# Optimization experiments

Hardware: AMD Instinct MI355X
Metric: run time of the kernel (lower is better)

## Reference

```python
import jax, jax.numpy as jnp
import numpy as np

DIM = 512
H = 48
W = 48
WS = 6
NH = 16
HEAD = DIM // NH
SCALE = HEAD ** -0.5
MLP_RATIO = 4
EPS = 1e-3  # keras LayerNormalization default epsilon
B = 16
L = H * W
M = WS * WS
NW = (H // WS) * (W // WS)


def _rel_pos_index(ws):
    # replicates tf.meshgrid (indexing='xy') construction exactly
    ch = np.arange(ws)
    cw = np.arange(ws)
    coords = np.stack(np.meshgrid(ch, cw))              # (2, ws, ws)
    cf = coords.reshape(2, -1)                          # (2, M)
    cf1 = np.concatenate([cf, np.zeros((2, 1), cf.dtype)], axis=1)  # (2, M+1) with global (0,0)
    rel = cf[:, :, None] - cf1[:, None, :]              # (2, M, M+1)
    rel = rel.transpose(1, 2, 0).copy()
    rel[:, :, 0] += ws - 1
    rel[:, :, 1] += ws - 1
    rel[:, :, 0] *= 2 * ws - 1
    return rel.sum(-1)                                  # (M, M+1)

REL_IDX = jnp.asarray(_rel_pos_index(WS))


def layernorm(x, g, b):
    m = x.mean(-1, keepdims=True)
    v = ((x - m) ** 2).mean(-1, keepdims=True)
    return (x - m) / jnp.sqrt(v + EPS) * g + b


def setup_inputs() -> dict:
    key = jax.random.key(0)
    ks = jax.random.split(key, 8)
    dense = lambda k, i, o: jax.random.normal(k, (i, o), jnp.float32) * (1.0 / np.sqrt(i))
    return dict(
        x=jax.random.normal(ks[0], (B, L, DIM), jnp.float32),
        xavg=jax.random.normal(ks[1], (B, 1, DIM), jnp.float32),
        w_kv=dense(ks[2], DIM, 2 * DIM), b_kv=jnp.zeros((2 * DIM,), jnp.float32),
        w_q=dense(ks[3], DIM, DIM), b_q=jnp.zeros((DIM,), jnp.float32),
        rel_bias_table=jax.random.normal(ks[4], ((2 * WS - 1) ** 2, NH), jnp.float32) * 0.02,
        g1=jnp.ones((DIM,), jnp.float32), be1=jnp.zeros((DIM,), jnp.float32),
        g2=jnp.ones((DIM,), jnp.float32), be2=jnp.zeros((DIM,), jnp.float32),
        w_fc1=dense(ks[5], DIM, MLP_RATIO * DIM), b_fc1=jnp.zeros((MLP_RATIO * DIM,), jnp.float32),
        w_fc2=dense(ks[6], MLP_RATIO * DIM, DIM), b_fc2=jnp.zeros((DIM,), jnp.float32),
    )


def _heads(t):
    # (B*, N, C) -> (B*, NH, N, HEAD)
    return t.reshape(t.shape[0], t.shape[1], NH, HEAD).transpose(0, 2, 1, 3)


def _forward(x, xavg, w_kv, b_kv, w_q, b_q, rel_bias_table, g1, be1, g2, be2,
             w_fc1, b_fc1, w_fc2, b_fc2):
    shortcut, shortcut_avg = x, xavg
    xn = layernorm(x, g1, be1)                          # (B, L, C)
    xavgn = layernorm(xavg, g1, be1)                    # (B, 1, C)

    # window partition: (B, L, C) -> (B*NW, M, C)
    xw = xn.reshape(B, H // WS, WS, W // WS, WS, DIM)
    xw = xw.transpose(0, 1, 3, 2, 4, 5).reshape(B * NW, M, DIM)

    # per-window tokens + repeated global token as keys/values
    xavgR = jnp.repeat(xavgn, NW, axis=0)               # (B*NW, 1, C), batch-major like tf.repeat
    x_c = jnp.concatenate([xw, xavgR], axis=1)          # (B*NW, M+1, C)

    kv = x_c @ w_kv + b_kv                              # (B*NW, M+1, 2C)
    q = xw @ w_q + b_q                                  # (B*NW, M, C)
    q_avg = xavgn @ w_q + b_q                           # (B, 1, C)
    kv_g = xn @ w_kv + b_kv                             # (B, L, 2C)

    k, v = jnp.split(kv, 2, axis=-1)
    kg, vg = jnp.split(kv_g, 2, axis=-1)

    qh = _heads(q) * SCALE                              # (B*NW, NH, M, HEAD)
    attn = jnp.einsum('bhqd,bhkd->bhqk', qh, _heads(k))  # (B*NW, NH, M, M+1)
    bias = rel_bias_table[REL_IDX.reshape(-1)].reshape(M, M + 1, NH)
    attn = attn + bias.transpose(2, 0, 1)[None]
    attn = jax.nn.softmax(attn, axis=-1)
    xo = jnp.einsum('bhqk,bhkd->bhqd', attn, _heads(v))
    xo = xo.transpose(0, 2, 1, 3).reshape(B * NW, M, DIM)

    # global token attends to all tokens
    qg = _heads(q_avg) * SCALE                          # (B, NH, 1, HEAD)
    attng = jax.nn.softmax(jnp.einsum('bhqd,bhkd->bhqk', qg, _heads(kg)), axis=-1)
    xavg_o = jnp.einsum('bhqk,bhkd->bhqd', attng, _heads(vg))
    xavg_o = xavg_o.transpose(0, 2, 1, 3).reshape(B, 1, DIM)

    # window reverse: (B*NW, M, C) -> (B, L, C)
    xr = xo.reshape(B, H // WS, W // WS, WS, WS, DIM)
    xr = xr.transpose(0, 1, 3, 2, 4, 5).reshape(B, L, DIM)

    x = shortcut + xr
    xavg = shortcut_avg + xavg_o

    mlp = lambda t: jax.nn.gelu(t @ w_fc1 + b_fc1, approximate=False) @ w_fc2 + b_fc2
    x = x + mlp(layernorm(x, g2, be2))
    xavg = xavg + mlp(layernorm(xavg, g2, be2))
    return x, xavg


def reference(x, xavg, w_kv, b_kv, w_q, b_q, rel_bias_table, g1, be1, g2, be2,
              w_fc1, b_fc1, w_fc2, b_fc2):
    return _forward(x, xavg, w_kv, b_kv, w_q, b_q, rel_bias_table, g1, be1, g2, be2,
                    w_fc1, b_fc1, w_fc2, b_fc2)
```

## Files before the change

kernel.cpp:

```cpp
#include <hip/hip_runtime.h>
#include <stdint.h>

#define DIM 512
#define NHEAD 16
#define HEADD 32
#define BATCH 16
#define SEQL 2304
#define XROWS (BATCH*SEQL)
#define NROWS (XROWS + BATCH)
#define ATT_SCALE 0.17677669529663687f

typedef __attribute__((ext_vector_type(8))) short short8;
typedef __attribute__((ext_vector_type(4))) float f32x4;

__device__ __forceinline__ float bf2f(unsigned short v) {
    union { unsigned u; float f; } t; t.u = ((unsigned)v) << 16; return t.f;
}
__device__ __forceinline__ unsigned short f2bf(float f) {
    union { float f; unsigned u; } t; t.f = f;
    unsigned r = t.u + 0x7fffu + ((t.u >> 16) & 1u);
    return (unsigned short)(r >> 16);
}
__device__ __forceinline__ void unpack8(const int4 c, float* o) {
    union { unsigned u; float f; } t;
    unsigned w0 = (unsigned)c.x, w1 = (unsigned)c.y, w2 = (unsigned)c.z, w3 = (unsigned)c.w;
    t.u = w0 << 16;         o[0] = t.f;
    t.u = w0 & 0xffff0000u; o[1] = t.f;
    t.u = w1 << 16;         o[2] = t.f;
    t.u = w1 & 0xffff0000u; o[3] = t.f;
    t.u = w2 << 16;         o[4] = t.f;
    t.u = w2 & 0xffff0000u; o[5] = t.f;
    t.u = w3 << 16;         o[6] = t.f;
    t.u = w3 & 0xffff0000u; o[7] = t.f;
}
__device__ __forceinline__ void gl_lds16(const void* g, void* l) {
    __builtin_amdgcn_global_load_lds((const __attribute__((address_space(1))) unsigned int*)g,
                                     (__attribute__((address_space(3))) unsigned int*)l,
                                     16, 0, 0);
}

__device__ __forceinline__ float gelu_exact(float v) {
    union { float f; unsigned u; } zc; zc.f = v * 0.70710678118654752f;
    unsigned sgn = zc.u & 0x80000000u;
    union { float f; unsigned u; } az; az.u = zc.u & 0x7fffffffu;
    float t  = __builtin_amdgcn_rcpf(fmaf(0.3275911f, az.f, 1.0f));
    float p  = t * fmaf(t, fmaf(t, fmaf(t, fmaf(t, 1.061405429f, -1.453152027f),
                                        1.421413741f), -0.284496736f), 0.254829592f);
    float e  = __expf(-az.f * az.f);
    union { float f; unsigned u; } er; er.f = fmaf(-p, e, 1.0f);
    er.u |= sgn;
    return 0.5f * v * (1.0f + er.f);
}

__device__ __forceinline__ void ln_row(const float* __restrict__ src, int lane,
                                       const float* __restrict__ g, const float* __restrict__ be,
                                       unsigned short* __restrict__ outrow) {
    int c0 = lane * 8;
    float4 v0 = *(const float4*)(src + c0);
    float4 v1 = *(const float4*)(src + c0 + 4);
    float s = v0.x+v0.y+v0.z+v0.w + v1.x+v1.y+v1.z+v1.w;
    float q = v0.x*v0.x+v0.y*v0.y+v0.z*v0.z+v0.w*v0.w + v1.x*v1.x+v1.y*v1.y+v1.z*v1.z+v1.w*v1.w;
    for (int m = 1; m < 64; m <<= 1) { s += __shfl_xor(s, m); q += __shfl_xor(q, m); }
    float mean = s * (1.0f/512.0f);
    float var  = q * (1.0f/512.0f) - mean*mean;
    float rs = rsqrtf(var + 1e-3f);
    float4 g0 = *(const float4*)(g + c0);
    float4 g1 = *(const float4*)(g + c0 + 4);
    float4 b0 = *(const float4*)(be + c0);
    float4 b1 = *(const float4*)(be + c0 + 4);
    unsigned short o[8];
    o[0] = f2bf((v0.x-mean)*rs*g0.x + b0.x);
    o[1] = f2bf((v0.y-mean)*rs*g0.y + b0.y);
    o[2] = f2bf((v0.z-mean)*rs*g0.z + b0.z);
    o[3] = f2bf((v0.w-mean)*rs*g0.w + b0.w);
    o[4] = f2bf((v1.x-mean)*rs*g1.x + b1.x);
    o[5] = f2bf((v1.y-mean)*rs*g1.y + b1.y);
    o[6] = f2bf((v1.z-mean)*rs*g1.z + b1.z);
    o[7] = f2bf((v1.w-mean)*rs*g1.w + b1.w);
    *(int4*)(outrow + c0) = *(const int4*)o;
}

#define TPOSE_BLKS 2816
#define SPACK_BLKS 90
#define LN1_BLKS   9220
__global__ __launch_bounds__(256) void prep_kernel(const float* __restrict__ w_q,
                                                   const float* __restrict__ w_kv,
                                                   const float* __restrict__ w_fc1,
                                                   const float* __restrict__ w_fc2,
                                                   unsigned short* __restrict__ Wqkv_t,
                                                   unsigned short* __restrict__ Wfc1_t,
                                                   unsigned short* __restrict__ Wfc2_t,
                                                   const float* __restrict__ b_q,
                                                   const float* __restrict__ b_kv,
                                                   const float* __restrict__ rel_table,
                                                   float* __restrict__ bqkv,
                                                   float* __restrict__ bias_exp,
                                                   const float* __restrict__ x,
                                                   const float* __restrict__ xavg,
                                                   const float* __restrict__ g1,
                                                   const float* __restrict__ be1,
                                                   unsigned short* __restrict__ xn) {
    __shared__ float tile[32][33];
    int blk = blockIdx.x;
    if (blk < TPOSE_BLKS) {
        int t = blk;
        const float* src; unsigned short* dst;
        int Kd, Nd, rowOff, tk;
        if (t < 256)        { src = w_q;   dst = Wqkv_t; Kd = 512;  Nd = 512;  rowOff = 0;   tk = 16; }
        else if (t < 768)   { t -= 256;  src = w_kv;  dst = Wqkv_t; Kd = 512;  Nd = 1024; rowOff = 512; tk = 16; }
        else if (t < 1792)  { t -= 768;  src = w_fc1; dst = Wfc1_t; Kd = 512;  Nd = 2048; rowOff = 0;   tk = 16; }
        else                { t -= 1792; src = w_fc2; dst = Wfc2_t; Kd = 2048; Nd = 512;  rowOff = 0;   tk = 64; }
        int k0 = (t % tk) * 32;
        int n0 = (t / tk) * 32;
        int tx = threadIdx.x & 31, ty = threadIdx.x >> 5;
        #pragma unroll
        for (int r = 0; r < 32; r += 8)
            tile[r + ty][tx] = src[(long)(k0 + r + ty) * Nd + n0 + tx];
        __syncthreads();
        #pragma unroll
        for (int r = 0; r < 32; r += 8)
            dst[(long)(rowOff + n0 + r + ty) * Kd + k0 + tx] = f2bf(tile[tx][r + ty]);
        return;
    }
    blk -= TPOSE_BLKS;
    if (blk < SPACK_BLKS) {
        int i = blk * 256 + threadIdx.x;
        if (i < 1536) { bqkv[i] = (i < 512) ? b_q[i] : b_kv[i - 512]; return; }
        i -= 1536;
        if (i < NHEAD*36*37) {
            int h = i / (36*37); int rem = i % (36*37); int qi = rem / 37; int j = rem % 37;
            int c0m = qi % 6, c1m = qi / 6;
            int c0n = (j < 36) ? (j % 6) : 0;
            int c1n = (j < 36) ? (j / 6) : 0;
            int id = (c0m - c0n + 5) * 11 + (c1m - c1n + 5);
            bias_exp[i] = rel_table[id * NHEAD + h];
        }
        return;
    }
    blk -= SPACK_BLKS;
    int wv = threadIdx.x >> 6, lane = threadIdx.x & 63;
    int r = blk * 4 + wv;
    if (r >= NROWS) return;
    const float* src = (r < XROWS) ? (x + (long)r * DIM) : (xavg + (long)(r - XROWS) * DIM);
    ln_row(src, lane, g1, be1, xn + (long)r * DIM);
}

__global__ __launch_bounds__(256) void ln_kernel(const float* __restrict__ p1,
                                                 const float* __restrict__ g, const float* __restrict__ be,
                                                 unsigned short* __restrict__ out, int nrows) {
    int wv = threadIdx.x >> 6, lane = threadIdx.x & 63;
    int r = blockIdx.x * 4 + wv;
    if (r >= nrows) return;
    ln_row(p1 + (long)r * DIM, lane, g, be, out + (long)r * DIM);
}

template<bool GELU_ACT, bool OUT_BF16, bool HAS_RES>
__global__ __launch_bounds__(256) void gemm_kernel(const short* __restrict__ A,
                                                   const short* __restrict__ Bt,
                                                   const float* __restrict__ bias,
                                                   void* __restrict__ Cout,
                                                   const float* __restrict__ Res,
                                                   int M, int N, int K, int nbx) {
    __shared__ short lds[2 * 128 * 64];
    short* lds_a = lds;
    short* lds_b = lds + 128 * 64;
    const int tid = threadIdx.x;
    const int lane = tid & 63;
    const int wv = tid >> 6;

    const int nwg = gridDim.x;
    const int orig = blockIdx.x;
    const int q = nwg >> 3, r = nwg & 7;
    const int xcd = orig & 7, lid = orig >> 3;
    const int wg = (xcd < r ? xcd * (q + 1) : r * (q + 1) + (xcd - r) * q) + lid;
    const int m0 = (wg / nbx) * 128;
    const int n0 = (wg % nbx) * 128;
    const int wm = (wv >> 1) * 64;
    const int wn = (wv & 1) * 64;

    f32x4 acc[4][4];
    #pragma unroll
    for (int i = 0; i < 4; i++)
        #pragma unroll
        for (int j = 0; j < 4; j++) { acc[i][j][0]=0.f; acc[i][j][1]=0.f; acc[i][j][2]=0.f; acc[i][j][3]=0.f; }

    const int srow = tid >> 3;
    const int msl  = (tid & 7) ^ (srow & 7);
    const short* Aa = A + (long)(m0 + srow) * K + msl * 8;
    const short* Bb = Bt + (long)(n0 + srow) * K + msl * 8;
    short* la = lds_a + tid * 8;
    short* lb = lds_b + tid * 8;

    const int quad = lane >> 4;
    const int l15 = lane & 15;
    const short* ra0 = lds_a + (wm + l15) * 64 + ((quad)     ^ (l15 & 7)) * 8;
    const short* ra1 = lds_a + (wm + l15) * 64 + ((4 + quad) ^ (l15 & 7)) * 8;
    const short* rb0 = lds_b + (wn + l15) * 64 + ((quad)     ^ (l15 & 7)) * 8;
    const short* rb1 = lds_b + (wn + l15) * 64 + ((4 + quad) ^ (l15 & 7)) * 8;

    for (int k0 = 0; k0 < K; k0 += 64) {
        __syncthreads();
        #pragma unroll
        for (int i = 0; i < 4; i++) {
            gl_lds16(Aa + (long)(i * 32) * K + k0, la + i * 256 * 8);
            gl_lds16(Bb + (long)(i * 32) * K + k0, lb + i * 256 * 8);
        }
        __syncthreads();
        short8 af[4], bf4[4];
        #pragma unroll
        for (int mt = 0; mt < 4; mt++) af[mt] = *(const short8*)(ra0 + mt * 16 * 64);
        #pragma unroll
        for (int nt = 0; nt < 4; nt++) bf4[nt] = *(const short8*)(rb0 + nt * 16 * 64);
        #pragma unroll
        for (int mt = 0; mt < 4; mt++)
            #pragma unroll
            for (int nt = 0; nt < 4; nt++)
                acc[mt][nt] = __builtin_amdgcn_mfma_f32_16x16x32_bf16(af[mt], bf4[nt], acc[mt][nt], 0, 0, 0);
        #pragma unroll
        for (int mt = 0; mt < 4; mt++) af[mt] = *(const short8*)(ra1 + mt * 16 * 64);
        #pragma unroll
        for (int nt = 0; nt < 4; nt++) bf4[nt] = *(const short8*)(rb1 + nt * 16 * 64);
        #pragma unroll
        for (int mt = 0; mt < 4; mt++)
            #pragma unroll
            for (int nt = 0; nt < 4; nt++)
                acc[mt][nt] = __builtin_amdgcn_mfma_f32_16x16x32_bf16(af[mt], bf4[nt], acc[mt][nt], 0, 0, 0);
    }

    float* ctile = (float*)lds;
    const int lrow_w = ((wv >> 1) << 4) + quad * 4;
    const int col_w  = ((wv & 1) << 6) + l15;
    const int lrow_r = tid >> 3;
    const int cg     = tid & 7;
    const int sub    = lrow_r & 15, half = lrow_r >> 4;
    float bv[16];
    #pragma unroll
    for (int i = 0; i < 4; i++)
        *(float4*)(bv + i * 4) = *(const float4*)(bias + n0 + cg * 16 + i * 4);

    #pragma unroll
    for (int mt = 0; mt < 4; mt++) {
        __syncthreads();
        #pragma unroll
        for (int nt = 0; nt < 4; nt++)
            #pragma unroll
            for (int r2 = 0; r2 < 4; r2++)
                ctile[(lrow_w + r2) * 132 + col_w + nt * 16] = acc[mt][nt][r2];
        __syncthreads();
        int grow = m0 + half * 64 + mt * 16 + sub;
        if (grow < M) {
            int gcol = n0 + cg * 16;
            float v[16];
            #pragma unroll
            for (int i = 0; i < 4; i++)
                *(float4*)(v + i * 4) = *(const float4*)(ctile + lrow_r * 132 + cg * 16 + i * 4);
            float rv[16];
            if (HAS_RES) {
                #pragma unroll
                for (int i = 0; i < 4; i++)
                    *(float4*)(rv + i * 4) = *(const float4*)(Res + (long)grow * N + gcol + i * 4);
            }
            if (OUT_BF16) {
                unsigned short ob[16];
                #pragma unroll
                for (int i = 0; i < 16; i++) {
                    float vv = v[i] + bv[i];
                    if (GELU_ACT) vv = gelu_exact(vv);
                    if (HAS_RES) vv += rv[i];
                    ob[i] = f2bf(vv);
                }
                unsigned short* dst = (unsigned short*)Cout + (long)grow * N + gcol;
                *(int4*)dst       = *(const int4*)ob;
                *(int4*)(dst + 8) = *(const int4*)(ob + 8);
            } else {
                float* dst = (float*)Cout + (long)grow * N + gcol;
                #pragma unroll
                for (int i = 0; i < 4; i++) {
                    float4 ov;
                    float* vp = v + i * 4;
                    float* rp = rv + i * 4;
                    ov.x = vp[0] + bv[i*4+0]; ov.y = vp[1] + bv[i*4+1];
                    ov.z = vp[2] + bv[i*4+2]; ov.w = vp[3] + bv[i*4+3];
                    if (GELU_ACT) { ov.x = gelu_exact(ov.x); ov.y = gelu_exact(ov.y);
                                    ov.z = gelu_exact(ov.z); ov.w = gelu_exact(ov.w); }
                    if (HAS_RES) { ov.x += rp[0]; ov.y += rp[1]; ov.z += rp[2]; ov.w += rp[3]; }
                    *(float4*)(dst + i * 4) = ov;
                }
            }
        }
    }
}

__global__ __launch_bounds__(256) void attn_kernel(const short* __restrict__ qkv,
                                                   const float* __restrict__ bias_exp,
                                                   const float* __restrict__ xin,
                                                   const float* __restrict__ xavg,
                                                   float* __restrict__ XALL) {
    __shared__ short vt[4][32 * 64];
    __shared__ short pl[4][48 * 64];
    __shared__ float sums[4][48];
    const int tid = threadIdx.x;
    if (blockIdx.x < 4096) {
        const int wv = tid >> 6;
        const int lane = tid & 63;
        const int gw = blockIdx.x * 4 + wv;
        const int win = gw >> 4;
        const int h = gw & 15;
        const int b = win >> 6;
        const int i1 = (win >> 3) & 7;
        const int i3 = win & 7;
        short* VT = vt[wv];
        short* PL = pl[wv];
        float* SM = sums[wv];
        const int quad = lane >> 4;
        const int l15 = lane & 15;

        {
            int4 z; z.x = 0; z.y = 0; z.z = 0; z.w = 0;
            int4* v4 = (int4*)VT;
            #pragma unroll
            for (int i = 0; i < 4; i++) v4[lane + 64 * i] = z;
            int4* p4 = (int4*)PL;
            #pragma unroll
            for (int i = 0; i < 6; i++) p4[lane + 64 * i] = z;
        }
        if (lane < 37) {
            long grow;
            if (lane < 36) { int i2 = lane / 6, i4 = lane % 6; grow = (long)b * SEQL + (i1*6 + i2) * 48 + i3*6 + i4; }
            else grow = XROWS + b;
            const int4* vp = (const int4*)(qkv + grow * 1536 + 1024 + h * 32);
            int4 r0 = vp[0], r1 = vp[1], r2v = vp[2], r3 = vp[3];
            const unsigned short* u0 = (const unsigned short*)&r0;
            const unsigned short* u1 = (const unsigned short*)&r1;
            const unsigned short* u2 = (const unsigned short*)&r2v;
            const unsigned short* u3 = (const unsigned short*)&r3;
            #pragma unroll
            for (int t = 0; t < 8; t++) VT[t * 64 + lane]        = (short)u0[t];
            #pragma unroll
            for (int t = 0; t < 8; t++) VT[(8 + t) * 64 + lane]  = (short)u1[t];
            #pragma unroll
            for (int t = 0; t < 8; t++) VT[(16 + t) * 64 + lane] = (short)u2[t];
            #pragma unroll
            for (int t = 0; t < 8; t++) VT[(24 + t) * 64 + lane] = (short)u3[t];
        }
        __syncthreads();

        short8 qf[3], kf[3];
        #pragma unroll
        for (int tm = 0; tm < 3; tm++) {
            int qi = tm * 16 + l15;
            if (qi < 36) {
                int i2 = qi / 6, i4 = qi % 6;
                long grow = (long)b * SEQL + (i1*6 + i2) * 48 + i3*6 + i4;
                qf[tm] = *(const short8*)(qkv + grow * 1536 + h * 32 + quad * 8);
            } else {
                #pragma unroll
                for (int i = 0; i < 8; i++) qf[tm][i] = 0;
            }
        }
        #pragma unroll
        for (int tn = 0; tn < 3; tn++) {
            int j = tn * 16 + l15;
            if (j <= 36) {
                long grow;
                if (j < 36) { int i2 = j / 6, i4 = j % 6; grow = (long)b * SEQL + (i1*6 + i2) * 48 + i3*6 + i4; }
                else grow = XROWS + b;
                kf[tn] = *(const short8*)(qkv + grow * 1536 + 512 + h * 32 + quad * 8);
            } else {
                #pragma unroll
                for (int i = 0; i < 8; i++) kf[tn][i] = 0;
            }
        }
        f32x4 s[3][3];
        #pragma unroll
        for (int tm = 0; tm < 3; tm++)
            #pragma unroll
            for (int tn = 0; tn < 3; tn++) {
                f32x4 z; z[0]=0.f; z[1]=0.f; z[2]=0.f; z[3]=0.f;
                s[tm][tn] = __builtin_amdgcn_mfma_f32_16x16x32_bf16(qf[tm], kf[tn], z, 0, 0, 0);
            }
        #pragma unroll
        for (int tm = 0; tm < 3; tm++)
            #pragma unroll
            for (int r = 0; r < 4; r++) {
                int qi = tm * 16 + quad * 4 + r;
                const float* bh = bias_exp + h * (36*37) + (qi < 36 ? qi : 35) * 37;
                #pragma unroll
                for (int tn = 0; tn < 3; tn++) {
                    int j = tn * 16 + l15;
                    float bv = bh[j <= 36 ? j : 36];
                    float v = fmaf(s[tm][tn][r], ATT_SCALE, bv);
                    s[tm][tn][r] = (j <= 36) ? v : -1e30f;
                }
            }
        #pragma unroll
        for (int tm = 0; tm < 3; tm++)
            #pragma unroll
            for (int r = 0; r < 4; r++) {
                float mx = fmaxf(fmaxf(s[tm][0][r], s[tm][1][r]), s[tm][2][r]);
                for (int m = 1; m < 16; m <<= 1) mx = fmaxf(mx, __shfl_xor(mx, m));
                float e0 = __expf(s[tm][0][r] - mx);
                float e1 = __expf(s[tm][1][r] - mx);
                float e2 = __expf(s[tm][2][r] - mx);
                float sum = e0 + e1 + e2;
                for (int m = 1; m < 16; m <<= 1) sum += __shfl_xor(sum, m);
                s[tm][0][r] = e0; s[tm][1][r] = e1; s[tm][2][r] = e2;
                if (l15 == 0) SM[tm * 16 + quad * 4 + r] = 1.0f / sum;
            }
        #pragma unroll
        for (int tm = 0; tm < 3; tm++)
            #pragma unroll
            for (int r = 0; r < 4; r++) {
                int row = (tm * 16 + quad * 4 + r) * 64;
                #pragma unroll
                for (int tn = 0; tn < 3; tn++)
                    PL[row + tn * 16 + l15] = (short)f2bf(s[tm][tn][r]);
            }
        f32x4 o[2][3];
        #pragma unroll
        for (int i = 0; i < 2; i++)
            #pragma unroll
            for (int j = 0; j < 3; j++) { o[i][j][0]=0.f; o[i][j][1]=0.f; o[i][j][2]=0.f; o[i][j][3]=0.f; }
        #pragma unroll
        for (int ch = 0; ch < 2; ch++) {
            short8 va[2], pb[3];
            #pragma unroll
            for (int tmd = 0; tmd < 2; tmd++)
                va[tmd] = *(const short8*)(VT + (tmd * 16 + l15) * 64 + ch * 32 + quad * 8);
            #pragma unroll
            for (int tnq = 0; tnq < 3; tnq++)
                pb[tnq] = *(const short8*)(PL + (tnq * 16 + l15) * 64 + ch * 32 + quad * 8);
            #pragma unroll
            for (int tmd = 0; tmd < 2; tmd++)
                #pragma unroll
                for (int tnq = 0; tnq < 3; tnq++)
                    o[tmd][tnq] = __builtin_amdgcn_mfma_f32_16x16x32_bf16(va[tmd], pb[tnq], o[tmd][tnq], 0, 0, 0);
        }
        #pragma unroll
        for (int tnq = 0; tnq < 3; tnq++) {
            int qi = tnq * 16 + l15;
            if (qi >= 36) continue;
            int i2 = qi / 6, i4 = qi % 6;
            long growq = (long)b * SEQL + (i1*6 + i2) * 48 + i3*6 + i4;
            float is = SM[qi];
            #pragma unroll
            for (int tmd = 0; tmd < 2; tmd++) {
                long base = growq * DIM + h * 32 + tmd * 16 + quad * 4;
                float4 xv = *(const float4*)(xin + base);
                float4 ov;
                ov.x = xv.x + o[tmd][tnq][0] * is;
                ov.y = xv.y + o[tmd][tnq][1] * is;
                ov.z = xv.z + o[tmd][tnq][2] * is;
                ov.w = xv.w + o[tmd][tnq][3] * is;
                *(float4*)(XALL + base) = ov;
            }
        }
        return;
    }
    {
        const int bb = blockIdx.x - 4096;
        const int b = bb >> 4;
        const int h = bb & 15;
        __shared__ float qs[32];
        __shared__ float redm[4], redsum[4];
        __shared__ float wout[4][32];
        if (tid < 32) qs[tid] = bf2f(((const unsigned short*)qkv)[(long)(XROWS + b) * 1536 + h * 32 + tid]);
        __syncthreads();
        float qr[32];
        #pragma unroll
        for (int d = 0; d < 32; d++) qr[d] = qs[d];
        float s[9];
        float mx = -1e30f;
        #pragma unroll
        for (int i = 0; i < 9; i++) {
            int t = tid + i * 256;
            const int4* kp = (const int4*)(qkv + (long)(b * SEQL + t) * 1536 + 512 + h * 32);
            float kr[32];
            unpack8(kp[0], kr); unpack8(kp[1], kr + 8); unpack8(kp[2], kr + 16); unpack8(kp[3], kr + 24);
            float d0 = 0.f, d1 = 0.f, d2 = 0.f, d3 = 0.f;
            #pragma unroll
            for (int dd = 0; dd < 8; dd++) {
                d0 += qr[dd] * kr[dd]; d1 += qr[8+dd] * kr[8+dd];
                d2 += qr[16+dd] * kr[16+dd]; d3 += qr[24+dd] * kr[24+dd];
            }
            s[i] = (d0 + d1 + d2 + d3) * ATT_SCALE;
            mx = fmaxf(mx, s[i]);
        }
        for (int m = 1; m < 64; m <<= 1) mx = fmaxf(mx, __shfl_xor(mx, m));
        if ((tid & 63) == 0) redm[tid >> 6] = mx;
        __syncthreads();
        mx = fmaxf(fmaxf(redm[0], redm[1]), fmaxf(redm[2], redm[3]));
        float sum = 0.f;
        #pragma unroll
        for (int i = 0; i < 9; i++) { s[i] = __expf(s[i] - mx); sum += s[i]; }
        for (int m = 1; m < 64; m <<= 1) sum += __shfl_xor(sum, m);
        if ((tid & 63) == 0) redsum[tid >> 6] = sum;
        __syncthreads();
        sum = redsum[0] + redsum[1] + redsum[2] + redsum[3];
        float o[32];
        #pragma unroll
        for (int d = 0; d < 32; d++) o[d] = 0.f;
        #pragma unroll
        for (int i = 0; i < 9; i++) {
            int t = tid + i * 256;
            const int4* vp = (const int4*)(qkv + (long)(b * SEQL + t) * 1536 + 1024 + h * 32);
            float vr[32];
            unpack8(vp[0], vr); unpack8(vp[1], vr + 8); unpack8(vp[2], vr + 16); unpack8(vp[3], vr + 24);
            float p = s[i];
            #pragma unroll
            for (int d = 0; d < 32; d++) o[d] += p * vr[d];
        }
        for (int m = 1; m < 64; m <<= 1) {
            #pragma unroll
            for (int d = 0; d < 32; d++) o[d] += __shfl_xor(o[d], m);
        }
        if ((tid & 63) == 0) {
            #pragma unroll
            for (int d = 0; d < 32; d++) wout[tid >> 6][d] = o[d];
        }
        __syncthreads();
        if (tid < 32) {
            float t = wout[0][tid] + wout[1][tid] + wout[2][tid] + wout[3][tid];
            XALL[(long)(XROWS + b) * DIM + h * 32 + tid] = xavg[b * DIM + h * 32 + tid] + t / sum;
        }
    }
}

extern "C" void kernel_launch(void* const* d_in, const int* in_sizes, int n_in,
                              void* d_out, int out_size, void* d_ws, size_t ws_size,
                              hipStream_t stream) {
    const float* x      = (const float*)d_in[0];
    const float* xavg   = (const float*)d_in[1];
    const float* w_kv   = (const float*)d_in[2];
    const float* b_kv   = (const float*)d_in[3];
    const float* w_q    = (const float*)d_in[4];
    const float* b_q    = (const float*)d_in[5];
    const float* rel    = (const float*)d_in[6];
    const float* g1     = (const float*)d_in[7];
    const float* be1    = (const float*)d_in[8];
    const float* g2     = (const float*)d_in[9];
    const float* be2    = (const float*)d_in[10];
    const float* w_fc1  = (const float*)d_in[11];
    const float* b_fc1  = (const float*)d_in[12];
    const float* w_fc2  = (const float*)d_in[13];
    const float* b_fc2  = (const float*)d_in[14];

    char* ws = (char*)d_ws;
    size_t off = 0;
    auto alloc = [&](size_t bytes) { void* p = ws + off; off += (bytes + 255) & ~(size_t)255; return p; };
    short* qkv_h          = (short*)alloc((size_t)NROWS * 2048 * 2);
    float* XALL           = (float*)alloc((size_t)NROWS * 512 * 4);
    short* xn             = (short*)alloc((size_t)NROWS * 512 * 2);
    unsigned short* Wqkv_t = (unsigned short*)alloc((size_t)1536 * 512 * 2);
    unsigned short* Wfc1_t = (unsigned short*)alloc((size_t)2048 * 512 * 2);
    unsigned short* Wfc2_t = (unsigned short*)alloc((size_t)512 * 2048 * 2);
    float* bqkv           = (float*)alloc(1536 * 4);
    float* bias_exp       = (float*)alloc((size_t)NHEAD * 36 * 37 * 4);

    const int MB = (NROWS + 127) / 128;

    prep_kernel<<<TPOSE_BLKS + SPACK_BLKS + LN1_BLKS, 256, 0, stream>>>(
        w_q, w_kv, w_fc1, w_fc2, Wqkv_t, Wfc1_t, Wfc2_t,
        b_q, b_kv, rel, bqkv, bias_exp,
        x, xavg, g1, be1, (unsigned short*)xn);
    gemm_kernel<false, true, false><<<12 * MB, 256, 0, stream>>>(
        xn, (const short*)Wqkv_t, bqkv, qkv_h, nullptr, NROWS, 1536, 512, 12);
    attn_kernel<<<4096 + 256, 256, 0, stream>>>(qkv_h, bias_exp, x, xavg, XALL);
    ln_kernel<<<(NROWS + 3) / 4, 256, 0, stream>>>(XALL, g2, be2, (unsigned short*)xn, NROWS);
    gemm_kernel<true, true, false><<<16 * MB, 256, 0, stream>>>(
        xn, (const short*)Wfc1_t, b_fc1, qkv_h, nullptr, NROWS, 2048, 512, 16);
    gemm_kernel<false, false, true><<<4 * MB, 256, 0, stream>>>(
        qkv_h, (const short*)Wfc2_t, b_fc2, d_out, XALL, NROWS, 512, 2048, 4);
}
```

Baseline: 677.1 us.

## Shrink attention blocks to two waves, add MFMA priority hints, direct-store fc2 epilogue

The attention kernel now launches 128-thread blocks holding two windows/heads each, doubling the block count. The global-token blocks process 18 tokens per thread instead of 9. s_setprio is raised around the MFMA sections. The GEMM gains an LDS_EPI template flag; the fc2 GEMM now writes results straight from accumulators to global memory, skipping the LDS staging and barriers, at the cost of uncoalesced scalar stores and residual loads.

Measured after the change: 753.3 us. 11.2% more time.

```diff
diff --git a/kernel.cpp b/kernel.cpp
--- a/kernel.cpp
+++ b/kernel.cpp
@@ -154,7 +154,7 @@
     ln_row(p1 + (long)r * DIM, lane, g, be, out + (long)r * DIM);
 }
 
-template<bool GELU_ACT, bool OUT_BF16, bool HAS_RES>
+template<bool GELU_ACT, bool OUT_BF16, bool HAS_RES, bool LDS_EPI>
 __global__ __launch_bounds__(256) void gemm_kernel(const short* __restrict__ A,
                                                    const short* __restrict__ Bt,
                                                    const float* __restrict__ bias,
@@ -227,83 +227,106 @@
                 acc[mt][nt] = __builtin_amdgcn_mfma_f32_16x16x32_bf16(af[mt], bf4[nt], acc[mt][nt], 0, 0, 0);
     }
 
-    float* ctile = (float*)lds;
-    const int lrow_w = ((wv >> 1) << 4) + quad * 4;
-    const int col_w  = ((wv & 1) << 6) + l15;
-    const int lrow_r = tid >> 3;
-    const int cg     = tid & 7;
-    const int sub    = lrow_r & 15, half = lrow_r >> 4;
-    float bv[16];
-    #pragma unroll
-    for (int i = 0; i < 4; i++)
-        *(float4*)(bv + i * 4) = *(const float4*)(bias + n0 + cg * 16 + i * 4);
-
-    #pragma unroll
-    for (int mt = 0; mt < 4; mt++) {
-        __syncthreads();
-        #pragma unroll
-        for (int nt = 0; nt < 4; nt++)
-            #pragma unroll
-            for (int r2 = 0; r2 < 4; r2++)
-                ctile[(lrow_w + r2) * 132 + col_w + nt * 16] = acc[mt][nt][r2];
-        __syncthreads();
-        int grow = m0 + half * 64 + mt * 16 + sub;
-        if (grow < M) {
-            int gcol = n0 + cg * 16;
-            float v[16];
-            #pragma unroll
-            for (int i = 0; i < 4; i++)
-                *(float4*)(v + i * 4) = *(const float4*)(ctile + lrow_r * 132 + cg * 16 + i * 4);
-            float rv[16];
-            if (HAS_RES) {
+    if (LDS_EPI) {
+        float* ctile = (float*)lds;
+        const int lrow_w = ((wv >> 1) << 4) + quad * 4;
+        const int col_w  = ((wv & 1) << 6) + l15;
+        const int lrow_r = tid >> 3;
+        const int cg     = tid & 7;
+        const int sub    = lrow_r & 15, half = lrow_r >> 4;
+        float bv[16];
+        #pragma unroll
+        for (int i = 0; i < 4; i++)
+            *(float4*)(bv + i * 4) = *(const float4*)(bias + n0 + cg * 16 + i * 4);
+
+        #pragma unroll
+        for (int mt = 0; mt < 4; mt++) {
+            __syncthreads();
+            #pragma unroll
+            for (int nt = 0; nt < 4; nt++)
+                #pragma unroll
+                for (int r2 = 0; r2 < 4; r2++)
+                    ctile[(lrow_w + r2) * 132 + col_w + nt * 16] = acc[mt][nt][r2];
+            __syncthreads();
+            int grow = m0 + half * 64 + mt * 16 + sub;
+            if (grow < M) {
+                int gcol = n0 + cg * 16;
+                float v[16];
                 #pragma unroll
                 for (int i = 0; i < 4; i++)
-                    *(float4*)(rv + i * 4) = *(const float4*)(Res + (long)grow * N + gcol + i * 4);
-            }
-            if (OUT_BF16) {
-                unsigned short ob[16];
-                #pragma unroll
-                for (int i = 0; i < 16; i++) {
-                    float vv = v[i] + bv[i];
-                    if (GELU_ACT) vv = gelu_exact(vv);
-                    if (HAS_RES) vv += rv[i];
-                    ob[i] = f2bf(vv);
+                    *(float4*)(v + i * 4) = *(const float4*)(ctile + lrow_r * 132 + cg * 16 + i * 4);
+                float rv[16];
+                if (HAS_RES) {
+                    #pragma unroll
+                    for (int i = 0; i < 4; i++)
+                        *(float4*)(rv + i * 4) = *(const float4*)(Res + (long)grow * N + gcol + i * 4);
                 }
-                unsigned short* dst = (unsigned short*)Cout + (long)grow * N + gcol;
-                *(int4*)dst       = *(const int4*)ob;
-                *(int4*)(dst + 8) = *(const int4*)(ob + 8);
-            } else {
-                float* dst = (float*)Cout + (long)grow * N + gcol;
-                #pragma unroll
-                for (int i = 0; i < 4; i++) {
-                    float4 ov;
-                    float* vp = v + i * 4;
-                    float* rp = rv + i * 4;
-                    ov.x = vp[0] + bv[i*4+0]; ov.y = vp[1] + bv[i*4+1];
-                    ov.z = vp[2] + bv[i*4+2]; ov.w = vp[3] + bv[i*4+3];
-                    if (GELU_ACT) { ov.x = gelu_exact(ov.x); ov.y = gelu_exact(ov.y);
-                                    ov.z = gelu_exact(ov.z); ov.w = gelu_exact(ov.w); }
-                    if (HAS_RES) { ov.x += rp[0]; ov.y += rp[1]; ov.z += rp[2]; ov.w += rp[3]; }
-                    *(float4*)(dst + i * 4) = ov;
+                if (OUT_BF16) {
+                    unsigned short ob[16];
+                    #pragma unroll
+                    for (int i = 0; i < 16; i++) {
+                        float vv = v[i] + bv[i];
+                        if (GELU_ACT) vv = gelu_exact(vv);
+                        if (HAS_RES) vv += rv[i];
+                        ob[i] = f2bf(vv);
+                    }
+                    unsigned short* dst = (unsigned short*)Cout + (long)grow * N + gcol;
+                    *(int4*)dst       = *(const int4*)ob;
+                    *(int4*)(dst + 8) = *(const int4*)(ob + 8);
+                } else {
+                    float* dst = (float*)Cout + (long)grow * N + gcol;
+                    #pragma unroll
+                    for (int i = 0; i < 4; i++) {
+                        float4 ov;
+                        float* vp = v + i * 4;
+                        float* rp = rv + i * 4;
+                        ov.x = vp[0] + bv[i*4+0]; ov.y = vp[1] + bv[i*4+1];
+                        ov.z = vp[2] + bv[i*4+2]; ov.w = vp[3] + bv[i*4+3];
+                        if (GELU_ACT) { ov.x = gelu_exact(ov.x); ov.y = gelu_exact(ov.y);
+                                        ov.z = gelu_exact(ov.z); ov.w = gelu_exact(ov.w); }
+                        if (HAS_RES) { ov.x += rp[0]; ov.y += rp[1]; ov.z += rp[2]; ov.w += rp[3]; }
+                        *(float4*)(dst + i * 4) = ov;
+                    }
                 }
             }
         }
+    } else {
+        #pragma unroll
+        for (int mt = 0; mt < 4; mt++) {
+            int rbase = m0 + wm + mt * 16 + quad * 4;
+            #pragma unroll
+            for (int nt = 0; nt < 4; nt++) {
+                int col = n0 + wn + nt * 16 + l15;
+                float bv = bias[col];
+                #pragma unroll
+                for (int r2 = 0; r2 < 4; r2++) {
+                    int row = rbase + r2;
+                    if (row < M) {
+                        float v = acc[mt][nt][r2] + bv;
+                        if (GELU_ACT) v = gelu_exact(v);
+                        if (HAS_RES) v += Res[(long)row * N + col];
+                        if (OUT_BF16) ((unsigned short*)Cout)[(long)row * N + col] = f2bf(v);
+                        else          ((float*)Cout)[(long)row * N + col] = v;
+                    }
+                }
+            }
+        }
     }
 }
 
-__global__ __launch_bounds__(256) void attn_kernel(const short* __restrict__ qkv,
+__global__ __launch_bounds__(128) void attn_kernel(const short* __restrict__ qkv,
                                                    const float* __restrict__ bias_exp,
                                                    const float* __restrict__ xin,
                                                    const float* __restrict__ xavg,
                                                    float* __restrict__ XALL) {
-    __shared__ short vt[4][32 * 64];
-    __shared__ short pl[4][48 * 64];
-    __shared__ float sums[4][48];
+    __shared__ short vt[2][32 * 64];
+    __shared__ short pl[2][48 * 64];
+    __shared__ float sums[2][48];
     const int tid = threadIdx.x;
-    if (blockIdx.x < 4096) {
+    if (blockIdx.x < 8192) {
         const int wv = tid >> 6;
         const int lane = tid & 63;
-        const int gw = blockIdx.x * 4 + wv;
+        const int gw = blockIdx.x * 2 + wv;
         const int win = gw >> 4;
         const int h = gw & 15;
         const int b = win >> 6;
@@ -372,6 +395,7 @@
             }
         }
         f32x4 s[3][3];
+        __builtin_amdgcn_s_setprio(1);
         #pragma unroll
         for (int tm = 0; tm < 3; tm++)
             #pragma unroll
@@ -379,6 +403,7 @@
                 f32x4 z; z[0]=0.f; z[1]=0.f; z[2]=0.f; z[3]=0.f;
                 s[tm][tn] = __builtin_amdgcn_mfma_f32_16x16x32_bf16(qf[tm], kf[tn], z, 0, 0, 0);
             }
+        __builtin_amdgcn_s_setprio(0);
         #pragma unroll
         for (int tm = 0; tm < 3; tm++)
             #pragma unroll
@@ -430,11 +455,13 @@
             #pragma unroll
             for (int tnq = 0; tnq < 3; tnq++)
                 pb[tnq] = *(const short8*)(PL + (tnq * 16 + l15) * 64 + ch * 32 + quad * 8);
+            __builtin_amdgcn_s_setprio(1);
             #pragma unroll
             for (int tmd = 0; tmd < 2; tmd++)
                 #pragma unroll
                 for (int tnq = 0; tnq < 3; tnq++)
                     o[tmd][tnq] = __builtin_amdgcn_mfma_f32_16x16x32_bf16(va[tmd], pb[tnq], o[tmd][tnq], 0, 0, 0);
+            __builtin_amdgcn_s_setprio(0);
         }
         #pragma unroll
         for (int tnq = 0; tnq < 3; tnq++) {
@@ -458,22 +485,22 @@
         return;
     }
     {
-        const int bb = blockIdx.x - 4096;
+        const int bb = blockIdx.x - 8192;
         const int b = bb >> 4;
         const int h = bb & 15;
         __shared__ float qs[32];
-        __shared__ float redm[4], redsum[4];
-        __shared__ float wout[4][32];
+        __shared__ float redm[2], redsum[2];
+        __shared__ float wout[2][32];
         if (tid < 32) qs[tid] = bf2f(((const unsigned short*)qkv)[(long)(XROWS + b) * 1536 + h * 32 + tid]);
         __syncthreads();
         float qr[32];
         #pragma unroll
         for (int d = 0; d < 32; d++) qr[d] = qs[d];
-        float s[9];
+        float s[18];
         float mx = -1e30f;
         #pragma unroll
-        for (int i = 0; i < 9; i++) {
-            int t = tid + i * 256;
+        for (int i = 0; i < 18; i++) {
+            int t = tid + i * 128;
             const int4* kp = (const int4*)(qkv + (long)(b * SEQL + t) * 1536 + 512 + h * 32);
             float kr[32];
             unpack8(kp[0], kr); unpack8(kp[1], kr + 8); unpack8(kp[2], kr + 16); unpack8(kp[3], kr + 24);
@@ -489,20 +516,20 @@
         for (int m = 1; m < 64; m <<= 1) mx = fmaxf(mx, __shfl_xor(mx, m));
         if ((tid & 63) == 0) redm[tid >> 6] = mx;
         __syncthreads();
-        mx = fmaxf(fmaxf(redm[0], redm[1]), fmaxf(redm[2], redm[3]));
+        mx = fmaxf(redm[0], redm[1]);
         float sum = 0.f;
         #pragma unroll
-        for (int i = 0; i < 9; i++) { s[i] = __expf(s[i] - mx); sum += s[i]; }
+        for (int i = 0; i < 18; i++) { s[i] = __expf(s[i] - mx); sum += s[i]; }
         for (int m = 1; m < 64; m <<= 1) sum += __shfl_xor(sum, m);
         if ((tid & 63) == 0) redsum[tid >> 6] = sum;
         __syncthreads();
-        sum = redsum[0] + redsum[1] + redsum[2] + redsum[3];
+        sum = redsum[0] + redsum[1];
         float o[32];
         #pragma unroll
         for (int d = 0; d < 32; d++) o[d] = 0.f;
         #pragma unroll
-        for (int i = 0; i < 9; i++) {
-            int t = tid + i * 256;
+        for (int i = 0; i < 18; i++) {
+            int t = tid + i * 128;
             const int4* vp = (const int4*)(qkv + (long)(b * SEQL + t) * 1536 + 1024 + h * 32);
             float vr[32];
             unpack8(vp[0], vr); unpack8(vp[1], vr + 8); unpack8(vp[2], vr + 16); unpack8(vp[3], vr + 24);
@@ -520,7 +547,7 @@
         }
         __syncthreads();
         if (tid < 32) {
-            float t = wout[0][tid] + wout[1][tid] + wout[2][tid] + wout[3][tid];
+            float t = wout[0][tid] + wout[1][tid];
             XALL[(long)(XROWS + b) * DIM + h * 32 + tid] = xavg[b * DIM + h * 32 + tid] + t / sum;
         }
     }
@@ -563,12 +590,12 @@
         w_q, w_kv, w_fc1, w_fc2, Wqkv_t, Wfc1_t, Wfc2_t,
         b_q, b_kv, rel, bqkv, bias_exp,
         x, xavg, g1, be1, (unsigned short*)xn);
-    gemm_kernel<false, true, false><<<12 * MB, 256, 0, stream>>>(
+    gemm_kernel<false, true, false, true><<<12 * MB, 256, 0, stream>>>(
         xn, (const short*)Wqkv_t, bqkv, qkv_h, nullptr, NROWS, 1536, 512, 12);
-    attn_kernel<<<4096 + 256, 256, 0, stream>>>(qkv_h, bias_exp, x, xavg, XALL);
+    attn_kernel<<<8192 + 256, 128, 0, stream>>>(qkv_h, bias_exp, x, xavg, XALL);
     ln_kernel<<<(NROWS + 3) / 4, 256, 0, stream>>>(XALL, g2, be2, (unsigned short*)xn, NROWS);
-    gemm_kernel<true, true, false><<<16 * MB, 256, 0, stream>>>(
+    gemm_kernel<true, true, false, true><<<16 * MB, 256, 0, stream>>>(
         xn, (const short*)Wfc1_t, b_fc1, qkv_h, nullptr, NROWS, 2048, 512, 16);
-    gemm_kernel<false, false, true><<<4 * MB, 256, 0, stream>>>(
+    gemm_kernel<false, false, true, false><<<4 * MB, 256, 0, stream>>>(
         qkv_h, (const short*)Wfc2_t, b_fc2, d_out, XALL, NROWS, 512, 2048, 4);
 }
```
